# Performance work log

Measured on AMD Instinct MI355X. Metric: run time of the kernel, lower is better.

The kernel has to match this reference:

```python
import jax, jax.numpy as jnp
import numpy as np


COMMITMENT_COST = 0.25


def setup_inputs() -> dict:
    key = jax.random.key(0)
    k1, k2 = jax.random.split(key)
    B, C, H, W = 16, 128, 64, 64
    K = 1024
    z = jax.random.normal(k1, (B, C, H, W), dtype=jnp.float32)
    # original init: uniform(-1/K, 1/K); keep that scale for faithfulness
    codebook = jax.random.uniform(k2, (K, C), dtype=jnp.float32,
                                  minval=-1.0 / K, maxval=1.0 / K)
    return {"z": z, "codebook": codebook}


def reference(z, codebook):
    B, C, H, W = z.shape
    K = codebook.shape[0]
    # (B,C,H,W) -> (N,C) with N = B*H*W
    z_flat = jnp.transpose(z, (0, 2, 3, 1)).reshape(-1, C)
    # squared-distance matrix (N,K): ||z||^2 + ||e||^2 - 2 z.e
    dists = (jnp.sum(z_flat ** 2, axis=1, keepdims=True)
             + jnp.sum(codebook ** 2, axis=1)
             - 2.0 * z_flat @ codebook.T)
    indices = jnp.argmin(dists, axis=1)  # (N,)
    z_q = jnp.transpose(codebook[indices].reshape(B, H, W, C), (0, 3, 1, 2))
    commitment_loss = jnp.mean((jax.lax.stop_gradient(z_q) - z) ** 2)
    codebook_loss = jnp.mean((z_q - jax.lax.stop_gradient(z)) ** 2)
    vq_loss = codebook_loss + COMMITMENT_COST * commitment_loss
    # straight-through estimator
    z_q_st = z + jax.lax.stop_gradient(z_q - z)
    usage = jnp.sum(jnp.bincount(indices, length=K) > 0).astype(jnp.float32) / K
    return (z_q_st, vq_loss, usage)
```

## Files before the change

### kernel.cpp

```cpp
#include <hip/hip_runtime.h>

typedef __attribute__((ext_vector_type(8))) short short8;
typedef __attribute__((ext_vector_type(4))) float f32x4;

#define C_DIM 128
#define K_CODES 1024
#define TOT 8388608
#define NBLK 512

__device__ __forceinline__ unsigned int f2bf1(float f) {
  unsigned int u = __float_as_uint(f);
  return (u + 0x7FFFu + ((u >> 16) & 1u)) >> 16;
}
__device__ __forceinline__ unsigned int f2bf2(float lo, float hi) {
  return f2bf1(lo) | (f2bf1(hi) << 16);
}

union U16x8 { uint4 u; short8 s; };

__global__ void prep_kernel(const float* __restrict__ cb,
                            unsigned short* __restrict__ ebf,
                            float* __restrict__ nsq1,
                            int* __restrict__ used) {
  int gid = blockIdx.x * 256 + threadIdx.x;
  ebf[gid] = (unsigned short)f2bf1(cb[gid]);
  if (gid < K_CODES) {
    float s = 0.f;
    #pragma unroll 8
    for (int c = 0; c < C_DIM; ++c) { float v = cb[gid * C_DIM + c]; s += v * v; }
    nsq1[gid] = 1.0f + s;
    used[gid] = 0;
  }
}

__global__ __launch_bounds__(256, 3)
void vq_main(const float* __restrict__ zin, const float* __restrict__ cb,
             const unsigned short* __restrict__ ebf,
             const float* __restrict__ nsq1,
             int* __restrict__ used, float* __restrict__ lossp,
             float* __restrict__ out) {
  __shared__ __align__(16) uint4 bG[2][1024];
  __shared__ float nsq_s[K_CODES];
  __shared__ unsigned int mergeK[128][2];
  __shared__ int   widx[128];
  __shared__ float wsum[4];

  const int t  = threadIdx.x;
  const int L  = t & 63;
  const int wv = t >> 6;
  const int ph = wv >> 1;
  const int kh = wv & 1;
  const int q  = L >> 4;
  const int nL = L & 15;

  const int bb = blockIdx.x >> 5;
  const int hg = blockIdx.x & 31;
  const int zoff = bb * (C_DIM * 4096) + hg * 128;

  for (int i = t; i < K_CODES; i += 256) nsq_s[i] = nsq1[i];

  short8 afrag[16];
  #pragma unroll
  for (int mt = 0; mt < 4; ++mt) {
    const int wcol = ph * 64 + mt * 16 + nL;
    #pragma unroll
    for (int ks = 0; ks < 4; ++ks) {
      float v[8];
      #pragma unroll
      for (int u = 0; u < 8; ++u)
        v[u] = zin[zoff + (ks * 32 + q * 8 + u) * 4096 + wcol];
      U16x8 pk;
      pk.u.x = f2bf2(-2.f * v[0], -2.f * v[1]);
      pk.u.y = f2bf2(-2.f * v[2], -2.f * v[3]);
      pk.u.z = f2bf2(-2.f * v[4], -2.f * v[5]);
      pk.u.w = f2bf2(-2.f * v[6], -2.f * v[7]);
      afrag[mt * 4 + ks] = pk.s;
    }
  }

  const uint4* __restrict__ ebv = (const uint4*)ebf;
  const int nLw = t >> 4;
  const int oct = t & 15;
  const int sks = oct >> 2, sq = oct & 3;

  #pragma unroll
  for (int p = 0; p < 4; ++p) {
    int r = p * 16 + nLw;
    bG[0][p * 256 + sks * 64 + nLw * 4 + sq] = ebv[r * 16 + oct];
  }
  __syncthreads();

  unsigned int kmin[16];
  #pragma unroll
  for (int i = 0; i < 16; ++i) kmin[i] = 0xFFFFFFFFu;

  #pragma unroll 1
  for (int ch = 0; ch < 16; ++ch) {
    const int cur = ch & 1;
    if (ch < 15) {
      #pragma unroll
      for (int p = 0; p < 4; ++p) {
        int r = p * 16 + nLw;
        bG[cur ^ 1][p * 256 + sks * 64 + nLw * 4 + sq] =
            ebv[((ch + 1) * 64 + r) * 16 + oct];
      }
    }
    const short8* bp = (const short8*)bG[cur];
    #pragma unroll
    for (int j2 = 0; j2 < 2; ++j2) {
      const int jj = kh * 2 + j2;
      const int row = ch * 64 + jj * 16 + nL;
      short8 b0 = bp[jj * 256 + 0 * 64 + nL * 4 + q];
      short8 b1 = bp[jj * 256 + 1 * 64 + nL * 4 + q];
      short8 b2 = bp[jj * 256 + 2 * 64 + nL * 4 + q];
      short8 b3 = bp[jj * 256 + 3 * 64 + nL * 4 + q];
      const float nv = nsq_s[row];
      f32x4 a0 = {nv, nv, nv, nv};
      f32x4 a1 = {nv, nv, nv, nv};
      f32x4 a2 = {nv, nv, nv, nv};
      f32x4 a3 = {nv, nv, nv, nv};
      a0 = __builtin_amdgcn_mfma_f32_16x16x32_bf16(afrag[0],  b0, a0, 0, 0, 0);
      a1 = __builtin_amdgcn_mfma_f32_16x16x32_bf16(afrag[4],  b0, a1, 0, 0, 0);
      a2 = __builtin_amdgcn_mfma_f32_16x16x32_bf16(afrag[8],  b0, a2, 0, 0, 0);
      a3 = __builtin_amdgcn_mfma_f32_16x16x32_bf16(afrag[12], b0, a3, 0, 0, 0);
      a0 = __builtin_amdgcn_mfma_f32_16x16x32_bf16(afrag[1],  b1, a0, 0, 0, 0);
      a1 = __builtin_amdgcn_mfma_f32_16x16x32_bf16(afrag[5],  b1, a1, 0, 0, 0);
      a2 = __builtin_amdgcn_mfma_f32_16x16x32_bf16(afrag[9],  b1, a2, 0, 0, 0);
      a3 = __builtin_amdgcn_mfma_f32_16x16x32_bf16(afrag[13], b1, a3, 0, 0, 0);
      a0 = __builtin_amdgcn_mfma_f32_16x16x32_bf16(afrag[2],  b2, a0, 0, 0, 0);
      a1 = __builtin_amdgcn_mfma_f32_16x16x32_bf16(afrag[6],  b2, a1, 0, 0, 0);
      a2 = __builtin_amdgcn_mfma_f32_16x16x32_bf16(afrag[10], b2, a2, 0, 0, 0);
      a3 = __builtin_amdgcn_mfma_f32_16x16x32_bf16(afrag[14], b2, a3, 0, 0, 0);
      a0 = __builtin_amdgcn_mfma_f32_16x16x32_bf16(afrag[3],  b3, a0, 0, 0, 0);
      a1 = __builtin_amdgcn_mfma_f32_16x16x32_bf16(afrag[7],  b3, a1, 0, 0, 0);
      a2 = __builtin_amdgcn_mfma_f32_16x16x32_bf16(afrag[11], b3, a2, 0, 0, 0);
      a3 = __builtin_amdgcn_mfma_f32_16x16x32_bf16(afrag[15], b3, a3, 0, 0, 0);
      const unsigned int rowc = (unsigned int)row;
      #pragma unroll
      for (int r = 0; r < 4; ++r) {
        unsigned int k0 = (__float_as_uint(a0[r]) & 0xFFFFFC00u) | rowc;
        if (k0 < kmin[r]) kmin[r] = k0;
        unsigned int k1 = (__float_as_uint(a1[r]) & 0xFFFFFC00u) | rowc;
        if (k1 < kmin[4 + r]) kmin[4 + r] = k1;
        unsigned int k2 = (__float_as_uint(a2[r]) & 0xFFFFFC00u) | rowc;
        if (k2 < kmin[8 + r]) kmin[8 + r] = k2;
        unsigned int k3 = (__float_as_uint(a3[r]) & 0xFFFFFC00u) | rowc;
        if (k3 < kmin[12 + r]) kmin[12 + r] = k3;
      }
    }
    __syncthreads();
  }

  #pragma unroll
  for (int m = 1; m <= 8; m <<= 1) {
    #pragma unroll
    for (int i = 0; i < 16; ++i) {
      unsigned int o = (unsigned int)__shfl_xor((int)kmin[i], m, 64);
      if (o < kmin[i]) kmin[i] = o;
    }
  }
  if (nL == 0) {
    #pragma unroll
    for (int mt = 0; mt < 4; ++mt)
      #pragma unroll
      for (int r = 0; r < 4; ++r)
        mergeK[ph * 64 + mt * 16 + q * 4 + r][kh] = kmin[mt * 4 + r];
  }
  __syncthreads();

  if (t < 128) {
    unsigned int b = min(mergeK[t][0], mergeK[t][1]);
    int bi = (int)(b & 1023u);
    widx[t] = bi;
    used[bi] = 1;
  }
  __syncthreads();

  float lsum = 0.f;
  {
    const int p = t & 127, cg = t >> 7;
    const int idx = widx[p];
    const uint4* erow = ebv + idx * 16 + cg * 8;
    const int obase = zoff + cg * 64 * 4096 + p;
    #pragma unroll 2
    for (int i = 0; i < 8; ++i) {
      uint4 g = erow[i];
      const unsigned int wrd[4] = {g.x, g.y, g.z, g.w};
      #pragma unroll
      for (int half = 0; half < 4; ++half) {
        float e0 = __uint_as_float(wrd[half] << 16);
        float e1 = __uint_as_float(wrd[half] & 0xFFFF0000u);
        int off = obase + (i * 8 + half * 2) * 4096;
        float d0 = zin[off] - e0;
        out[off] = e0;
        lsum += d0 * d0;
        off += 4096;
        float d1 = zin[off] - e1;
        out[off] = e1;
        lsum += d1 * d1;
      }
    }
  }
  #pragma unroll
  for (int o = 32; o > 0; o >>= 1) lsum += __shfl_down(lsum, o, 64);
  if (L == 0) wsum[wv] = lsum;
  __syncthreads();
  if (t == 0) lossp[blockIdx.x] = wsum[0] + wsum[1] + wsum[2] + wsum[3];
}

__global__ void finalize_kernel(const int* __restrict__ used,
                                const float* __restrict__ lossp,
                                float* __restrict__ out2) {
  __shared__ int   redi[256];
  __shared__ float redf[256];
  int t = threadIdx.x;
  int s = 0;
  for (int i = t; i < K_CODES; i += 256) s += (used[i] != 0) ? 1 : 0;
  float ls = 0.f;
  for (int i = t; i < NBLK; i += 256) ls += lossp[i];
  redi[t] = s; redf[t] = ls;
  __syncthreads();
  for (int o = 128; o > 0; o >>= 1) {
    if (t < o) { redi[t] += redi[t + o]; redf[t] += redf[t + o]; }
    __syncthreads();
  }
  if (t == 0) {
    out2[0] = 1.25f * redf[0] / (float)TOT;
    out2[1] = (float)redi[0] / 1024.0f;
  }
}

extern "C" void kernel_launch(void* const* d_in, const int* in_sizes, int n_in,
                              void* d_out, int out_size, void* d_ws, size_t ws_size,
                              hipStream_t stream) {
  const float* z  = (const float*)d_in[0];
  const float* cb = (const float*)d_in[1];
  float* out = (float*)d_out;
  char* ws = (char*)d_ws;
  unsigned short* ebf = (unsigned short*)ws;
  float* nsq1  = (float*)(ws + 262144);
  int*   used  = (int*)(ws + 266240);
  float* lossp = (float*)(ws + 270336);

  hipLaunchKernelGGL(prep_kernel, dim3(512), dim3(256), 0, stream,
                     cb, ebf, nsq1, used);
  hipLaunchKernelGGL(vq_main, dim3(NBLK), dim3(256), 0, stream,
                     z, cb, ebf, nsq1, used, lossp, out);
  hipLaunchKernelGGL(finalize_kernel, dim3(1), dim3(256), 0, stream,
                     used, lossp, out + TOT);
}
```

Before: 116.0 us.

## Use 512-thread blocks with 8 waves splitting pixels, and vectorize codebook bf16 prep

The main kernel now runs 8 wavefronts per block instead of 4. Each wave handles 32 pixels instead of 64, which halves the A fragments and the min-key registers per thread, and the codebook staging, epilogue and loss reduction are split across the extra waves. This aims to raise latency hiding and occupancy on a grid of only 512 blocks, at the cost of each wave reusing every B fragment over fewer MFMAs. The prep kernel now converts four floats per thread with float4 loads and launches fewer blocks.

```diff
diff --git a/kernel.cpp b/kernel.cpp
--- a/kernel.cpp
+++ b/kernel.cpp
@@ -23,18 +23,22 @@
                             float* __restrict__ nsq1,
                             int* __restrict__ used) {
   int gid = blockIdx.x * 256 + threadIdx.x;
-  ebf[gid] = (unsigned short)f2bf1(cb[gid]);
+  const float4 v = ((const float4*)cb)[gid];
+  uint2 pk;
+  pk.x = f2bf2(v.x, v.y);
+  pk.y = f2bf2(v.z, v.w);
+  ((uint2*)ebf)[gid] = pk;
   if (gid < K_CODES) {
     float s = 0.f;
     #pragma unroll 8
-    for (int c = 0; c < C_DIM; ++c) { float v = cb[gid * C_DIM + c]; s += v * v; }
+    for (int c = 0; c < C_DIM; ++c) { float w = cb[gid * C_DIM + c]; s += w * w; }
     nsq1[gid] = 1.0f + s;
     used[gid] = 0;
   }
 }
 
-__global__ __launch_bounds__(256, 3)
-void vq_main(const float* __restrict__ zin, const float* __restrict__ cb,
+__global__ __launch_bounds__(512, 4)
+void vq_main(const float* __restrict__ zin,
              const unsigned short* __restrict__ ebf,
              const float* __restrict__ nsq1,
              int* __restrict__ used, float* __restrict__ lossp,
@@ -43,7 +47,7 @@
   __shared__ float nsq_s[K_CODES];
   __shared__ unsigned int mergeK[128][2];
   __shared__ int   widx[128];
-  __shared__ float wsum[4];
+  __shared__ float wsum[8];
 
   const int t  = threadIdx.x;
   const int L  = t & 63;
@@ -57,12 +61,12 @@
   const int hg = blockIdx.x & 31;
   const int zoff = bb * (C_DIM * 4096) + hg * 128;
 
-  for (int i = t; i < K_CODES; i += 256) nsq_s[i] = nsq1[i];
-
-  short8 afrag[16];
-  #pragma unroll
-  for (int mt = 0; mt < 4; ++mt) {
-    const int wcol = ph * 64 + mt * 16 + nL;
+  for (int i = t; i < K_CODES; i += 512) nsq_s[i] = nsq1[i];
+
+  short8 afrag[8];
+  #pragma unroll
+  for (int mt = 0; mt < 2; ++mt) {
+    const int wcol = ph * 32 + mt * 16 + nL;
     #pragma unroll
     for (int ks = 0; ks < 4; ++ks) {
       float v[8];
@@ -79,30 +83,31 @@
   }
 
   const uint4* __restrict__ ebv = (const uint4*)ebf;
-  const int nLw = t >> 4;
+  const int nLw = (t >> 4) & 15;
   const int oct = t & 15;
+  const int pb  = t >> 8;
   const int sks = oct >> 2, sq = oct & 3;
 
   #pragma unroll
-  for (int p = 0; p < 4; ++p) {
-    int r = p * 16 + nLw;
-    bG[0][p * 256 + sks * 64 + nLw * 4 + sq] = ebv[r * 16 + oct];
-  }
-  __syncthreads();
-
-  unsigned int kmin[16];
-  #pragma unroll
-  for (int i = 0; i < 16; ++i) kmin[i] = 0xFFFFFFFFu;
+  for (int i = 0; i < 2; ++i) {
+    int p = pb + 2 * i;
+    bG[0][p * 256 + sks * 64 + nLw * 4 + sq] = ebv[(p * 16 + nLw) * 16 + oct];
+  }
+  __syncthreads();
+
+  unsigned int kmin[8];
+  #pragma unroll
+  for (int i = 0; i < 8; ++i) kmin[i] = 0xFFFFFFFFu;
 
   #pragma unroll 1
   for (int ch = 0; ch < 16; ++ch) {
     const int cur = ch & 1;
     if (ch < 15) {
       #pragma unroll
-      for (int p = 0; p < 4; ++p) {
-        int r = p * 16 + nLw;
+      for (int i = 0; i < 2; ++i) {
+        int p = pb + 2 * i;
         bG[cur ^ 1][p * 256 + sks * 64 + nLw * 4 + sq] =
-            ebv[((ch + 1) * 64 + r) * 16 + oct];
+            ebv[((ch + 1) * 64 + p * 16 + nLw) * 16 + oct];
       }
     }
     const short8* bp = (const short8*)bG[cur];
@@ -115,37 +120,23 @@
       short8 b2 = bp[jj * 256 + 2 * 64 + nL * 4 + q];
       short8 b3 = bp[jj * 256 + 3 * 64 + nL * 4 + q];
       const float nv = nsq_s[row];
-      f32x4 a0 = {nv, nv, nv, nv};
-      f32x4 a1 = {nv, nv, nv, nv};
-      f32x4 a2 = {nv, nv, nv, nv};
-      f32x4 a3 = {nv, nv, nv, nv};
-      a0 = __builtin_amdgcn_mfma_f32_16x16x32_bf16(afrag[0],  b0, a0, 0, 0, 0);
-      a1 = __builtin_amdgcn_mfma_f32_16x16x32_bf16(afrag[4],  b0, a1, 0, 0, 0);
-      a2 = __builtin_amdgcn_mfma_f32_16x16x32_bf16(afrag[8],  b0, a2, 0, 0, 0);
-      a3 = __builtin_amdgcn_mfma_f32_16x16x32_bf16(afrag[12], b0, a3, 0, 0, 0);
-      a0 = __builtin_amdgcn_mfma_f32_16x16x32_bf16(afrag[1],  b1, a0, 0, 0, 0);
-      a1 = __builtin_amdgcn_mfma_f32_16x16x32_bf16(afrag[5],  b1, a1, 0, 0, 0);
-      a2 = __builtin_amdgcn_mfma_f32_16x16x32_bf16(afrag[9],  b1, a2, 0, 0, 0);
-      a3 = __builtin_amdgcn_mfma_f32_16x16x32_bf16(afrag[13], b1, a3, 0, 0, 0);
-      a0 = __builtin_amdgcn_mfma_f32_16x16x32_bf16(afrag[2],  b2, a0, 0, 0, 0);
-      a1 = __builtin_amdgcn_mfma_f32_16x16x32_bf16(afrag[6],  b2, a1, 0, 0, 0);
-      a2 = __builtin_amdgcn_mfma_f32_16x16x32_bf16(afrag[10], b2, a2, 0, 0, 0);
-      a3 = __builtin_amdgcn_mfma_f32_16x16x32_bf16(afrag[14], b2, a3, 0, 0, 0);
-      a0 = __builtin_amdgcn_mfma_f32_16x16x32_bf16(afrag[3],  b3, a0, 0, 0, 0);
-      a1 = __builtin_amdgcn_mfma_f32_16x16x32_bf16(afrag[7],  b3, a1, 0, 0, 0);
-      a2 = __builtin_amdgcn_mfma_f32_16x16x32_bf16(afrag[11], b3, a2, 0, 0, 0);
-      a3 = __builtin_amdgcn_mfma_f32_16x16x32_bf16(afrag[15], b3, a3, 0, 0, 0);
+      f32x4 c0 = {nv, nv, nv, nv};
+      f32x4 c1 = {nv, nv, nv, nv};
+      c0 = __builtin_amdgcn_mfma_f32_16x16x32_bf16(afrag[0], b0, c0, 0, 0, 0);
+      c1 = __builtin_amdgcn_mfma_f32_16x16x32_bf16(afrag[4], b0, c1, 0, 0, 0);
+      c0 = __builtin_amdgcn_mfma_f32_16x16x32_bf16(afrag[1], b1, c0, 0, 0, 0);
+      c1 = __builtin_amdgcn_mfma_f32_16x16x32_bf16(afrag[5], b1, c1, 0, 0, 0);
+      c0 = __builtin_amdgcn_mfma_f32_16x16x32_bf16(afrag[2], b2, c0, 0, 0, 0);
+      c1 = __builtin_amdgcn_mfma_f32_16x16x32_bf16(afrag[6], b2, c1, 0, 0, 0);
+      c0 = __builtin_amdgcn_mfma_f32_16x16x32_bf16(afrag[3], b3, c0, 0, 0, 0);
+      c1 = __builtin_amdgcn_mfma_f32_16x16x32_bf16(afrag[7], b3, c1, 0, 0, 0);
       const unsigned int rowc = (unsigned int)row;
       #pragma unroll
       for (int r = 0; r < 4; ++r) {
-        unsigned int k0 = (__float_as_uint(a0[r]) & 0xFFFFFC00u) | rowc;
+        unsigned int k0 = (__float_as_uint(c0[r]) & 0xFFFFFC00u) | rowc;
         if (k0 < kmin[r]) kmin[r] = k0;
-        unsigned int k1 = (__float_as_uint(a1[r]) & 0xFFFFFC00u) | rowc;
+        unsigned int k1 = (__float_as_uint(c1[r]) & 0xFFFFFC00u) | rowc;
         if (k1 < kmin[4 + r]) kmin[4 + r] = k1;
-        unsigned int k2 = (__float_as_uint(a2[r]) & 0xFFFFFC00u) | rowc;
-        if (k2 < kmin[8 + r]) kmin[8 + r] = k2;
-        unsigned int k3 = (__float_as_uint(a3[r]) & 0xFFFFFC00u) | rowc;
-        if (k3 < kmin[12 + r]) kmin[12 + r] = k3;
       }
     }
     __syncthreads();
@@ -154,17 +145,17 @@
   #pragma unroll
   for (int m = 1; m <= 8; m <<= 1) {
     #pragma unroll
-    for (int i = 0; i < 16; ++i) {
+    for (int i = 0; i < 8; ++i) {
       unsigned int o = (unsigned int)__shfl_xor((int)kmin[i], m, 64);
       if (o < kmin[i]) kmin[i] = o;
     }
   }
   if (nL == 0) {
     #pragma unroll
-    for (int mt = 0; mt < 4; ++mt)
+    for (int mt = 0; mt < 2; ++mt)
       #pragma unroll
       for (int r = 0; r < 4; ++r)
-        mergeK[ph * 64 + mt * 16 + q * 4 + r][kh] = kmin[mt * 4 + r];
+        mergeK[ph * 32 + mt * 16 + q * 4 + r][kh] = kmin[mt * 4 + r];
   }
   __syncthreads();
 
@@ -180,10 +171,10 @@
   {
     const int p = t & 127, cg = t >> 7;
     const int idx = widx[p];
-    const uint4* erow = ebv + idx * 16 + cg * 8;
-    const int obase = zoff + cg * 64 * 4096 + p;
-    #pragma unroll 2
-    for (int i = 0; i < 8; ++i) {
+    const uint4* erow = ebv + idx * 16 + cg * 4;
+    const int obase = zoff + cg * 32 * 4096 + p;
+    #pragma unroll
+    for (int i = 0; i < 4; ++i) {
       uint4 g = erow[i];
       const unsigned int wrd[4] = {g.x, g.y, g.z, g.w};
       #pragma unroll
@@ -205,7 +196,9 @@
   for (int o = 32; o > 0; o >>= 1) lsum += __shfl_down(lsum, o, 64);
   if (L == 0) wsum[wv] = lsum;
   __syncthreads();
-  if (t == 0) lossp[blockIdx.x] = wsum[0] + wsum[1] + wsum[2] + wsum[3];
+  if (t == 0)
+    lossp[blockIdx.x] = ((wsum[0] + wsum[1]) + (wsum[2] + wsum[3]))
+                      + ((wsum[4] + wsum[5]) + (wsum[6] + wsum[7]));
 }
 
 __global__ void finalize_kernel(const int* __restrict__ used,
@@ -242,10 +235,10 @@
   int*   used  = (int*)(ws + 266240);
   float* lossp = (float*)(ws + 270336);
 
-  hipLaunchKernelGGL(prep_kernel, dim3(512), dim3(256), 0, stream,
+  hipLaunchKernelGGL(prep_kernel, dim3(128), dim3(256), 0, stream,
                      cb, ebf, nsq1, used);
-  hipLaunchKernelGGL(vq_main, dim3(NBLK), dim3(256), 0, stream,
-                     z, cb, ebf, nsq1, used, lossp, out);
+  hipLaunchKernelGGL(vq_main, dim3(NBLK), dim3(512), 0, stream,
+                     z, ebf, nsq1, used, lossp, out);
   hipLaunchKernelGGL(finalize_kernel, dim3(1), dim3(256), 0, stream,
                      used, lossp, out + TOT);
 }
```

Result: no change. 116.9 us (+0.8%).

## Derive loss from min distance, swizzle LDS codebook tiles, vectorize prep

Applied to the files above, without the earlier changes.

Computes the loss as ||z||^2 plus the selected argmin distance, using the (1+||e||^2 - 2z·e) value packed into the key, instead of re-reading z in the output pass. This removes a second full read of the 32 MB input. It also XOR-swizzles the LDS layout of the bf16 codebook tiles to cut bank conflicts, and vectorizes bf16 conversion in prep with 4x fewer blocks. The risk is precision: the distance is a bf16 MFMA result with its low mantissa bits masked, so the loss can drift from the exact fp32 value.

```diff
diff --git a/kernel.cpp b/kernel.cpp
--- a/kernel.cpp
+++ b/kernel.cpp
@@ -23,18 +23,22 @@
                             float* __restrict__ nsq1,
                             int* __restrict__ used) {
   int gid = blockIdx.x * 256 + threadIdx.x;
-  ebf[gid] = (unsigned short)f2bf1(cb[gid]);
+  const float4 v = ((const float4*)cb)[gid];
+  uint2 pk;
+  pk.x = f2bf2(v.x, v.y);
+  pk.y = f2bf2(v.z, v.w);
+  ((uint2*)ebf)[gid] = pk;
   if (gid < K_CODES) {
     float s = 0.f;
     #pragma unroll 8
-    for (int c = 0; c < C_DIM; ++c) { float v = cb[gid * C_DIM + c]; s += v * v; }
+    for (int c = 0; c < C_DIM; ++c) { float w = cb[gid * C_DIM + c]; s += w * w; }
     nsq1[gid] = 1.0f + s;
     used[gid] = 0;
   }
 }
 
 __global__ __launch_bounds__(256, 3)
-void vq_main(const float* __restrict__ zin, const float* __restrict__ cb,
+void vq_main(const float* __restrict__ zin,
              const unsigned short* __restrict__ ebf,
              const float* __restrict__ nsq1,
              int* __restrict__ used, float* __restrict__ lossp,
@@ -60,6 +64,7 @@
   for (int i = t; i < K_CODES; i += 256) nsq_s[i] = nsq1[i];
 
   short8 afrag[16];
+  float zsq = 0.f;
   #pragma unroll
   for (int mt = 0; mt < 4; ++mt) {
     const int wcol = ph * 64 + mt * 16 + nL;
@@ -67,8 +72,10 @@
     for (int ks = 0; ks < 4; ++ks) {
       float v[8];
       #pragma unroll
-      for (int u = 0; u < 8; ++u)
+      for (int u = 0; u < 8; ++u) {
         v[u] = zin[zoff + (ks * 32 + q * 8 + u) * 4096 + wcol];
+        zsq += v[u] * v[u];
+      }
       U16x8 pk;
       pk.u.x = f2bf2(-2.f * v[0], -2.f * v[1]);
       pk.u.y = f2bf2(-2.f * v[2], -2.f * v[3]);
@@ -77,18 +84,23 @@
       afrag[mt * 4 + ks] = pk.s;
     }
   }
+  zsq = (kh == 0) ? zsq : 0.f;
 
   const uint4* __restrict__ ebv = (const uint4*)ebf;
   const int nLw = t >> 4;
   const int oct = t & 15;
   const int sks = oct >> 2, sq = oct & 3;
-
-  #pragma unroll
-  for (int p = 0; p < 4; ++p) {
-    int r = p * 16 + nLw;
-    bG[0][p * 256 + sks * 64 + nLw * 4 + sq] = ebv[r * 16 + oct];
-  }
-  __syncthreads();
+  const int swbase = (nLw >> 1) * 8 + (((nLw ^ sks) & 1) << 2)
+                   + ((sq ^ (nLw >> 1)) & 3);
+
+  #pragma unroll
+  for (int p = 0; p < 4; ++p)
+    bG[0][p * 256 + sks * 64 + swbase] = ebv[(p * 16 + nLw) * 16 + oct];
+  __syncthreads();
+
+  const int rdq = (q ^ (nL >> 1)) & 3;
+  const int sA = (nL >> 1) * 8 + ((nL & 1) << 2) + rdq;
+  const int sB = (nL >> 1) * 8 + (((nL ^ 1) & 1) << 2) + rdq;
 
   unsigned int kmin[16];
   #pragma unroll
@@ -99,21 +111,19 @@
     const int cur = ch & 1;
     if (ch < 15) {
       #pragma unroll
-      for (int p = 0; p < 4; ++p) {
-        int r = p * 16 + nLw;
-        bG[cur ^ 1][p * 256 + sks * 64 + nLw * 4 + sq] =
-            ebv[((ch + 1) * 64 + r) * 16 + oct];
-      }
+      for (int p = 0; p < 4; ++p)
+        bG[cur ^ 1][p * 256 + sks * 64 + swbase] =
+            ebv[((ch + 1) * 64 + p * 16 + nLw) * 16 + oct];
     }
     const short8* bp = (const short8*)bG[cur];
     #pragma unroll
     for (int j2 = 0; j2 < 2; ++j2) {
       const int jj = kh * 2 + j2;
       const int row = ch * 64 + jj * 16 + nL;
-      short8 b0 = bp[jj * 256 + 0 * 64 + nL * 4 + q];
-      short8 b1 = bp[jj * 256 + 1 * 64 + nL * 4 + q];
-      short8 b2 = bp[jj * 256 + 2 * 64 + nL * 4 + q];
-      short8 b3 = bp[jj * 256 + 3 * 64 + nL * 4 + q];
+      short8 b0 = bp[jj * 256 +   0 + sA];
+      short8 b1 = bp[jj * 256 +  64 + sB];
+      short8 b2 = bp[jj * 256 + 128 + sA];
+      short8 b3 = bp[jj * 256 + 192 + sB];
       const float nv = nsq_s[row];
       f32x4 a0 = {nv, nv, nv, nv};
       f32x4 a1 = {nv, nv, nv, nv};
@@ -168,21 +178,22 @@
   }
   __syncthreads();
 
+  float dval = 0.f;
   if (t < 128) {
     unsigned int b = min(mergeK[t][0], mergeK[t][1]);
     int bi = (int)(b & 1023u);
     widx[t] = bi;
     used[bi] = 1;
-  }
-  __syncthreads();
-
-  float lsum = 0.f;
+    dval = __uint_as_float(b & 0xFFFFFC00u) - 1.0f;
+  }
+  __syncthreads();
+
   {
     const int p = t & 127, cg = t >> 7;
     const int idx = widx[p];
     const uint4* erow = ebv + idx * 16 + cg * 8;
     const int obase = zoff + cg * 64 * 4096 + p;
-    #pragma unroll 2
+    #pragma unroll
     for (int i = 0; i < 8; ++i) {
       uint4 g = erow[i];
       const unsigned int wrd[4] = {g.x, g.y, g.z, g.w};
@@ -191,21 +202,19 @@
         float e0 = __uint_as_float(wrd[half] << 16);
         float e1 = __uint_as_float(wrd[half] & 0xFFFF0000u);
         int off = obase + (i * 8 + half * 2) * 4096;
-        float d0 = zin[off] - e0;
         out[off] = e0;
-        lsum += d0 * d0;
-        off += 4096;
-        float d1 = zin[off] - e1;
-        out[off] = e1;
-        lsum += d1 * d1;
+        out[off + 4096] = e1;
       }
     }
   }
+
+  float lsum = zsq + dval;
   #pragma unroll
   for (int o = 32; o > 0; o >>= 1) lsum += __shfl_down(lsum, o, 64);
   if (L == 0) wsum[wv] = lsum;
   __syncthreads();
-  if (t == 0) lossp[blockIdx.x] = wsum[0] + wsum[1] + wsum[2] + wsum[3];
+  if (t == 0)
+    lossp[blockIdx.x] = (wsum[0] + wsum[1]) + (wsum[2] + wsum[3]);
 }
 
 __global__ void finalize_kernel(const int* __restrict__ used,
@@ -242,10 +251,10 @@
   int*   used  = (int*)(ws + 266240);
   float* lossp = (float*)(ws + 270336);
 
-  hipLaunchKernelGGL(prep_kernel, dim3(512), dim3(256), 0, stream,
+  hipLaunchKernelGGL(prep_kernel, dim3(128), dim3(256), 0, stream,
                      cb, ebf, nsq1, used);
   hipLaunchKernelGGL(vq_main, dim3(NBLK), dim3(256), 0, stream,
-                     z, cb, ebf, nsq1, used, lossp, out);
+                     z, ebf, nsq1, used, lossp, out);
   hipLaunchKernelGGL(finalize_kernel, dim3(1), dim3(256), 0, stream,
                      used, lossp, out + TOT);
 }
```

Result: slower. 136.2 us (+17.4%).
